# Performance work log

Hardware: AMD Instinct MI355X
Metric: run time of the kernel (lower is better)

The kernel has to match this reference:

```python
import jax, jax.numpy as jnp
import numpy as np

D_MODEL = 2048
N_HEADS = 16
HEAD_DIM = D_MODEL // N_HEADS
LN_EPS = 1e-6  # flax.linen.LayerNorm default
NEG_INF = float('-inf')


def _layernorm_scale_only(x, scale):
    # flax LayerNorm with use_bias=False: normalize over last axis, scale only
    mean = jnp.mean(x, axis=-1, keepdims=True)
    var = jnp.var(x, axis=-1, keepdims=True)
    return (x - mean) * jax.lax.rsqrt(var + LN_EPS) * scale


def setup_inputs() -> dict:
    key = jax.random.key(0)
    ks = jax.random.split(key, 4)
    B, S = 2, 2048
    x = jax.random.normal(ks[0], (B, S, D_MODEL), dtype=jnp.float32)
    Wqkv = jax.random.normal(ks[1], (D_MODEL, 3 * D_MODEL), dtype=jnp.float32) * 0.02
    q_ln_scale = jnp.ones((D_MODEL,), dtype=jnp.float32)
    k_ln_scale = jnp.ones((D_MODEL,), dtype=jnp.float32)
    out_W = jax.random.normal(ks[2], (D_MODEL, D_MODEL), dtype=jnp.float32) * 0.02
    return {"x": x, "Wqkv": Wqkv, "q_ln_scale": q_ln_scale,
            "k_ln_scale": k_ln_scale, "out_W": out_W}


def reference(x, Wqkv, q_ln_scale, k_ln_scale, out_W):
    B, S, _ = x.shape
    qkv = jnp.einsum('bsd,de->bse', x, Wqkv)  # [B,S,3*D] (no bias)
    q, k, v = jnp.split(qkv, 3, axis=-1)
    # QK LayerNorm (attn_qk_ln=True, no bias)
    q = _layernorm_scale_only(q, q_ln_scale)
    k = _layernorm_scale_only(k, k_ln_scale)
    # split heads: [B,S,H,Dh]
    q = q.reshape(B, S, N_HEADS, HEAD_DIM)
    k = k.reshape(B, S, N_HEADS, HEAD_DIM)
    v = v.reshape(B, S, N_HEADS, HEAD_DIM)
    # scaled scores [B,H,S,S]
    scores = jnp.einsum('bshd,bthd->bhst', q / jnp.sqrt(jnp.float32(HEAD_DIM)), k)
    # causal mask: triu(ones, k=1) marks strictly-future positions -> -inf
    causal = jnp.triu(jnp.ones((S, S), dtype=bool), 1)
    scores = jnp.where(causal, NEG_INF, scores)
    # kv-cache mask: arange(S) < S - past_position - S = 0 -> all False (no-op
    # with past_position=0 and no layer_past), faithfully omitted.
    attn = jax.nn.softmax(scores, axis=-1)
    ctx = jnp.einsum('bhst,bthd->bshd', attn, v)  # [B,S,H,Dh]
    out = jnp.einsum('bsd,de->bse', ctx.reshape(B, S, D_MODEL), out_W)
    return out
```

## Files before the change

kernel.cpp:

```cpp
#include <hip/hip_runtime.h>


typedef float f32x4 __attribute__((ext_vector_type(4)));
typedef short s16x8 __attribute__((ext_vector_type(8)));
typedef short s16x4 __attribute__((ext_vector_type(4)));

static __device__ __forceinline__ unsigned short f2bf(float f) {
  unsigned u = __builtin_bit_cast(unsigned, f);
  unsigned r = u + 0x7fffu + ((u >> 16) & 1u);
  return (unsigned short)(r >> 16);
}
static __device__ __forceinline__ float bf2f(unsigned short s) {
  unsigned u = ((unsigned)s) << 16;
  return __builtin_bit_cast(float, u);
}

static __device__ __forceinline__ void gload_lds16(const unsigned short* g, unsigned short* l) {
  __builtin_amdgcn_global_load_lds((const __attribute__((address_space(1))) void*)g,
                                   (__attribute__((address_space(3))) void*)l, 16, 0, 0);
}

__global__ __launch_bounds__(256) void k_cvt4(const float4* __restrict__ in,
                                              s16x4* __restrict__ out, int n) {
  int i = blockIdx.x * 256 + threadIdx.x;
  if (i >= n) return;
  float4 v = in[i];
  s16x4 o = { (short)f2bf(v.x), (short)f2bf(v.y), (short)f2bf(v.z), (short)f2bf(v.w) };
  out[i] = o;
}

__global__ __launch_bounds__(256) void k_twT(const float* __restrict__ in,
                                             unsigned short* __restrict__ out,
                                             int K, int N) {
  __shared__ float tile[32][33];
  const int n0 = blockIdx.x * 32, k0 = blockIdx.y * 32;
  const int tx = threadIdx.x & 31, ty = threadIdx.x >> 5;
#pragma unroll
  for (int rr = 0; rr < 4; ++rr) {
    int kr = ty + rr * 8;
    tile[kr][tx] = in[(size_t)(k0 + kr) * N + n0 + tx];
  }
  __syncthreads();
#pragma unroll
  for (int rr = 0; rr < 4; ++rr) {
    int nr = ty + rr * 8;
    out[(size_t)(n0 + nr) * K + k0 + tx] = f2bf(tile[tx][nr]);
  }
}

template <int BF16OUT>
__global__ __launch_bounds__(256) void k_gemm(const unsigned short* __restrict__ A,
                                              const unsigned short* __restrict__ Bt,
                                              void* __restrict__ Cout,
                                              int M, int N, int K) {
  __shared__ unsigned short sA[128 * 32];
  __shared__ unsigned short sB[128 * 32];
  const int t = threadIdx.x;
  const int w = t >> 6, lane = t & 63, g = lane >> 4, l15 = lane & 15;
  const int m0 = blockIdx.y * 128, n0 = blockIdx.x * 128;
  const int wm = (w >> 1) * 64, wn = (w & 1) * 64;
  f32x4 acc[4][4];
#pragma unroll
  for (int i = 0; i < 4; i++)
#pragma unroll
    for (int j = 0; j < 4; j++) acc[i][j] = (f32x4){0.f, 0.f, 0.f, 0.f};

  const int nk = K >> 5;
  for (int kt = 0; kt < nk; ++kt) {
    __syncthreads();
#pragma unroll
    for (int it = 0; it < 2; ++it) {
      int flat = it * 256 + t;
      int row = flat >> 2, ch = flat & 3;
      gload_lds16(A  + (size_t)(m0 + row) * K + kt * 32 + ch * 8,
                  sA + (size_t)(it * 256 + w * 64) * 8);
      gload_lds16(Bt + (size_t)(n0 + row) * K + kt * 32 + ch * 8,
                  sB + (size_t)(it * 256 + w * 64) * 8);
    }
    __syncthreads();
    s16x8 af[4], bf[4];
#pragma unroll
    for (int i = 0; i < 4; i++) {
      af[i] = *(const s16x8*)&sA[(wm + i * 16 + l15) * 32 + 8 * g];
      bf[i] = *(const s16x8*)&sB[(wn + i * 16 + l15) * 32 + 8 * g];
    }
#pragma unroll
    for (int i = 0; i < 4; i++)
#pragma unroll
      for (int j = 0; j < 4; j++)
        acc[i][j] = __builtin_amdgcn_mfma_f32_16x16x32_bf16(af[i], bf[j], acc[i][j], 0, 0, 0);
  }
#pragma unroll
  for (int i = 0; i < 4; i++) {
#pragma unroll
    for (int j = 0; j < 4; j++) {
#pragma unroll
      for (int r = 0; r < 4; r++) {
        int row = m0 + wm + i * 16 + 4 * g + r;
        int col = n0 + wn + j * 16 + l15;
        if (BF16OUT)
          ((unsigned short*)Cout)[(size_t)row * N + col] = f2bf(acc[i][j][r]);
        else
          ((float*)Cout)[(size_t)row * N + col] = acc[i][j][r];
      }
    }
  }
}

__global__ __launch_bounds__(256) void k_ln(unsigned short* __restrict__ qkv,
                                            const float* __restrict__ qsc,
                                            const float* __restrict__ ksc) {
  __shared__ float red[8];
  const int t = threadIdx.x;
  const int w = t >> 6;
  unsigned short* base = qkv + (size_t)blockIdx.x * 6144;
#pragma unroll
  for (int part = 0; part < 2; ++part) {
    unsigned short* p = base + part * 2048 + t * 8;
    s16x8 v = *(const s16x8*)p;
    float f[8], s = 0.f, q = 0.f;
#pragma unroll
    for (int j = 0; j < 8; j++) { f[j] = bf2f((unsigned short)v[j]); s += f[j]; q += f[j] * f[j]; }
#pragma unroll
    for (int m = 1; m < 64; m <<= 1) { s += __shfl_xor(s, m); q += __shfl_xor(q, m); }
    __syncthreads();
    if ((t & 63) == 0) { red[w] = s; red[4 + w] = q; }
    __syncthreads();
    s = red[0] + red[1] + red[2] + red[3];
    q = red[4] + red[5] + red[6] + red[7];
    float mean = s * (1.f / 2048.f);
    float var = q * (1.f / 2048.f) - mean * mean;
    float inv = rsqrtf(var + 1e-6f);
    const float* sc = part ? ksc : qsc;
    float extra = part ? 1.0f : 0.12751743f;
    s16x8 o;
#pragma unroll
    for (int j = 0; j < 8; j++) o[j] = (short)f2bf((f[j] - mean) * inv * (sc[t * 8 + j] * extra));
    *(s16x8*)p = o;
  }
}

__global__ __launch_bounds__(256) void k_vT(const unsigned short* __restrict__ qkv,
                                            unsigned short* __restrict__ vt) {
  __shared__ unsigned short tl[64][136];
  const int bh = blockIdx.y;
  const int b = bh >> 4, h = bh & 15;
  const int s0 = blockIdx.x * 64;
  const int t = threadIdx.x;
#pragma unroll
  for (int it = 0; it < 4; ++it) {
    int flat = it * 256 + t;
    int r = flat >> 4, c = flat & 15;
    s16x8 v = *(const s16x8*)(qkv + (size_t)(b * 2048 + s0 + r) * 6144 + 4096 + h * 128 + c * 8);
    *((s16x8*)&tl[r][c * 8]) = v;
  }
  __syncthreads();
#pragma unroll
  for (int it = 0; it < 4; ++it) {
    int flat = it * 256 + t;
    int d = flat >> 3, cs = flat & 7;
    s16x8 o;
#pragma unroll
    for (int e = 0; e < 8; e++) {
      int key = (cs >> 2) * 32 + (e >> 2) * 16 + (cs & 3) * 4 + (e & 3);
      o[e] = (short)tl[key][d];
    }
    *(s16x8*)(vt + (size_t)(bh * 128 + d) * 2048 + s0 + cs * 8) = o;
  }
}

__global__ __launch_bounds__(256) void k_attn(const unsigned short* __restrict__ qkv,
                                              const unsigned short* __restrict__ vt,
                                              unsigned short* __restrict__ ctx) {
  __shared__ unsigned short sK[2][64 * 128];
  __shared__ unsigned short sV[2][128 * 64];
  const int t = threadIdx.x;
  const int w = t >> 6, lane = t & 63, g = lane >> 4, l15 = lane & 15;
  const int pair = blockIdx.x, h = blockIdx.y, b = blockIdx.z;
  const int qt0 = 31 - pair, qt1 = pair;
  const int n0 = qt0 + 1;
  const int NT = 33;
  const unsigned short* kbase = qkv + (size_t)(b * 2048) * 6144 + 2048 + h * 128;
  const unsigned short* vbase = vt + (size_t)((b * 16 + h) * 128) * 2048;

  auto issue_kv = [&](int k0, int bufi) {
#pragma unroll
    for (int it2 = 0; it2 < 4; ++it2) {
      int flat = it2 * 256 + t;
      int r = flat >> 4, c = flat & 15;
      gload_lds16(kbase + (size_t)(k0 + r) * 6144 + ((c ^ (r & 15)) * 8),
                  (unsigned short*)&sK[bufi][(it2 * 256 + w * 64) * 8]);
    }
#pragma unroll
    for (int it2 = 0; it2 < 4; ++it2) {
      int flat = it2 * 256 + t;
      int d = flat >> 3, z = flat & 7;
      gload_lds16(vbase + (size_t)d * 2048 + k0 + ((z ^ (d & 7)) * 8),
                  (unsigned short*)&sV[bufi][(it2 * 256 + w * 64) * 8]);
    }
  };

  s16x8 bq[4];
  auto load_q = [&](int q0) {
#pragma unroll
    for (int ks = 0; ks < 4; ++ks)
      bq[ks] = *(const s16x8*)(qkv + (size_t)(b * 2048 + q0 + w * 16 + l15) * 6144 +
                               h * 128 + (ks * 4 + g) * 8);
  };

  f32x4 o[8];
  float mrun, lrun;
  auto reset_state = [&]() {
#pragma unroll
    for (int nd = 0; nd < 8; ++nd) o[nd] = (f32x4){0.f, 0.f, 0.f, 0.f};
    mrun = -INFINITY; lrun = 0.f;
  };
  auto write_o = [&](int q0) {
    float ivr[4];
#pragma unroll
    for (int r = 0; r < 4; ++r) ivr[r] = 1.0f / __shfl(lrun, 4 * g + r);
#pragma unroll
    for (int nd = 0; nd < 8; ++nd) {
      const int col = h * 128 + nd * 16 + l15;
#pragma unroll
      for (int r = 0; r < 4; ++r) {
        const int row = b * 2048 + q0 + w * 16 + 4 * g + r;
        ctx[(size_t)row * 2048 + col] = f2bf(o[nd][r] * ivr[r]);
      }
    }
  };

  reset_state();
  load_q(qt0 * 64);
  issue_kv(0, 0);
  int cur = 0;

  for (int it = 0; it < NT; ++it) {
    const int seg = (it < n0) ? 0 : 1;
    const int qt = seg ? qt1 : qt0;
    const int kt = seg ? it - n0 : it;

    if (it + 1 < NT) {
      const int kn = (it + 1 < n0) ? it + 1 : it + 1 - n0;
      issue_kv(kn * 64, cur ^ 1);
      asm volatile("s_waitcnt vmcnt(8)" ::: "memory");
    } else {
      asm volatile("s_waitcnt vmcnt(0)" ::: "memory");
    }
    __builtin_amdgcn_sched_barrier(0);
    __builtin_amdgcn_s_barrier();

    if (seg == 1 && kt == 0) {
      write_o(qt0 * 64);
      reset_state();
      load_q(qt1 * 64);
    }

    const unsigned short* sKc = &sK[cur][0];
    const unsigned short* sVc = &sV[cur][0];

    f32x4 st[4];
#pragma unroll
    for (int mi = 0; mi < 4; ++mi) st[mi] = (f32x4){0.f, 0.f, 0.f, 0.f};
#pragma unroll
    for (int mi = 0; mi < 4; ++mi) {
#pragma unroll
      for (int ks = 0; ks < 4; ++ks) {
        s16x8 ak = *(const s16x8*)&sKc[(mi * 16 + l15) * 128 + (((ks * 4 + g) ^ l15) * 8)];
        st[mi] = __builtin_amdgcn_mfma_f32_16x16x32_bf16(ak, bq[ks], st[mi], 0, 0, 0);
      }
    }

    if (kt == qt) {
      const int qloc = w * 16 + l15;
#pragma unroll
      for (int mi = 0; mi < 4; ++mi)
#pragma unroll
        for (int r = 0; r < 4; ++r)
          if (mi * 16 + 4 * g + r > qloc) st[mi][r] = -INFINITY;
    }

    float mt = -INFINITY;
#pragma unroll
    for (int mi = 0; mi < 4; ++mi)
#pragma unroll
      for (int r = 0; r < 4; ++r) mt = fmaxf(mt, st[mi][r]);
    mt = fmaxf(mt, __shfl_xor(mt, 16));
    mt = fmaxf(mt, __shfl_xor(mt, 32));

    if (!__all(mt <= mrun + 8.f)) {
      const float mnew = fmaxf(mrun, mt);
      const float alpha = exp2f(mrun - mnew);
      lrun *= alpha;
      float ar[4];
#pragma unroll
      for (int r = 0; r < 4; ++r) ar[r] = __shfl(alpha, 4 * g + r);
#pragma unroll
      for (int nd = 0; nd < 8; ++nd)
#pragma unroll
        for (int r = 0; r < 4; ++r) o[nd][r] *= ar[r];
      mrun = mnew;
    }

    float ls = 0.f;
#pragma unroll
    for (int mi = 0; mi < 4; ++mi)
#pragma unroll
      for (int r = 0; r < 4; ++r) {
        float pp = exp2f(st[mi][r] - mrun);
        st[mi][r] = pp;
        ls += pp;
      }
    ls += __shfl_xor(ls, 16);
    ls += __shfl_xor(ls, 32);
    lrun += ls;

    s16x8 pa01, pa23;
#pragma unroll
    for (int j = 0; j < 8; ++j) {
      pa01[j] = (short)f2bf(st[j >> 2][j & 3]);
      pa23[j] = (short)f2bf(st[2 + (j >> 2)][j & 3]);
    }

#pragma unroll
    for (int nd = 0; nd < 8; ++nd) {
      const int d = nd * 16 + l15;
      const int zs = d & 7;
      s16x8 bv0 = *(const s16x8*)&sVc[d * 64 + ((g ^ zs) * 8)];
      s16x8 bv1 = *(const s16x8*)&sVc[d * 64 + (((4 + g) ^ zs) * 8)];
      o[nd] = __builtin_amdgcn_mfma_f32_16x16x32_bf16(pa01, bv0, o[nd], 0, 0, 0);
      o[nd] = __builtin_amdgcn_mfma_f32_16x16x32_bf16(pa23, bv1, o[nd], 0, 0, 0);
    }

    __builtin_amdgcn_sched_barrier(0);
    __builtin_amdgcn_s_barrier();
    cur ^= 1;
  }
  write_o(qt1 * 64);
}

extern "C" void kernel_launch(void* const* d_in, const int* in_sizes, int n_in,
                              void* d_out, int out_size, void* d_ws, size_t ws_size,
                              hipStream_t stream) {
  (void)in_sizes; (void)n_in; (void)out_size; (void)ws_size;
  const float* x    = (const float*)d_in[0];
  const float* Wqkv = (const float*)d_in[1];
  const float* qsc  = (const float*)d_in[2];
  const float* ksc  = (const float*)d_in[3];
  const float* outW = (const float*)d_in[4];

  char* ws = (char*)d_ws;
  unsigned short* xb  = (unsigned short*)(ws);
  unsigned short* wT  = (unsigned short*)(ws + 16777216);
  unsigned short* owT = (unsigned short*)(ws + 41943040);
  unsigned short* qkv = (unsigned short*)(ws + 50331648);
  unsigned short* vt  = (unsigned short*)(ws + 100663296);
  unsigned short* ctx = xb;

  k_cvt4<<<8192, 256, 0, stream>>>((const float4*)x, (s16x4*)xb, 2097152);
  k_twT<<<dim3(192, 64), 256, 0, stream>>>(Wqkv, wT, 2048, 6144);
  k_twT<<<dim3(64, 64), 256, 0, stream>>>(outW, owT, 2048, 2048);
  k_gemm<1><<<dim3(48, 32), 256, 0, stream>>>(xb, wT, (void*)qkv, 4096, 6144, 2048);
  k_ln<<<4096, 256, 0, stream>>>(qkv, qsc, ksc);
  k_vT<<<dim3(32, 32), 256, 0, stream>>>(qkv, vt);
  k_attn<<<dim3(16, 16, 2), 256, 0, stream>>>(qkv, vt, ctx);
  k_gemm<0><<<dim3(16, 32), 256, 0, stream>>>(ctx, owT, d_out, 4096, 2048, 2048);
}
```

Measured before the change: 317.2 us.

## Replace QKV projection GEMM with 256x256 tiled, 8-wave pipelined MFMA kernel

Adds a new bf16 GEMM kernel for the QKV projection. It uses 256x256 output tiles, 512 threads, double-buffered 64-wide K stages loaded directly into XOR-swizzled LDS, and interleaved quarter-tile MFMA phases with explicit waitcnt, barriers and setprio. An XCD-aware block swizzle remaps the 384 blocks. The goal is more data reuse per LDS load and overlap of global loads with compute, replacing the 128x128 kernel. The cost is heavy register pressure and fragile hand-tuned vmcnt counts.

After: 303.1 us. -4.5%, faster.

```diff
diff --git a/kernel.cpp b/kernel.cpp
--- a/kernel.cpp
+++ b/kernel.cpp
@@ -46,6 +46,165 @@
     int nr = ty + rr * 8;
     out[(size_t)(n0 + nr) * K + k0 + tx] = f2bf(tile[tx][nr]);
   }
+}
+
+__global__ __launch_bounds__(512, 2) void k_gemm256(const unsigned short* __restrict__ A,
+                                                    const unsigned short* __restrict__ Bt,
+                                                    unsigned short* __restrict__ Cout,
+                                                    int N, int K, int nbn) {
+  __shared__ unsigned short sA[2 * 2 * 128 * 64];
+  __shared__ unsigned short sB[2 * 2 * 128 * 64];
+  const int t = threadIdx.x;
+  const int wid = t >> 6, lane = t & 63, g = lane >> 4, l15 = lane & 15;
+  const int wm2 = wid >> 2, wn2 = wid & 3;
+  const int xr = l15 & 7;
+
+  const int cpx = (int)gridDim.x >> 3;
+  const int swz = ((int)blockIdx.x & 7) * cpx + ((int)blockIdx.x >> 3);
+  const int m0 = (swz / nbn) * 256, n0 = (swz % nbn) * 256;
+
+  const int srow = t >> 3;
+  const int sslot = (t & 7) ^ (srow & 7);
+  const unsigned short* pA = A  + (size_t)(m0 + srow) * K + sslot * 8;
+  const unsigned short* pB = Bt + (size_t)(n0 + srow) * K + sslot * 8;
+  const int ldsb = wid * 512;
+
+  auto stageA = [&](int kt, int h) {
+#pragma unroll
+    for (int j = 0; j < 2; ++j)
+      gload_lds16(pA + (size_t)(h * 128 + j * 64) * K + kt * 64,
+                  sA + ((kt & 1) * 2 + h) * 8192 + j * 4096 + ldsb);
+  };
+  auto stageB = [&](int kt, int h) {
+#pragma unroll
+    for (int j = 0; j < 2; ++j)
+      gload_lds16(pB + (size_t)(h * 128 + j * 64) * K + kt * 64,
+                  sB + ((kt & 1) * 2 + h) * 8192 + j * 4096 + ldsb);
+  };
+
+  const int arow = wm2 * 64 + l15;
+  const int brow = wn2 * 32 + l15;
+  const int sl0 = (g ^ xr) * 8, sl1 = ((4 + g) ^ xr) * 8;
+
+  f32x4 acc[2][2][4][2];
+#pragma unroll
+  for (int a = 0; a < 2; ++a)
+#pragma unroll
+    for (int b = 0; b < 2; ++b)
+#pragma unroll
+      for (int c = 0; c < 4; ++c)
+#pragma unroll
+        for (int d = 0; d < 2; ++d) acc[a][b][c][d] = (f32x4){0.f, 0.f, 0.f, 0.f};
+
+  const int NK = K >> 6;
+  stageA(0, 0); stageB(0, 0); stageB(0, 1); stageA(0, 1); stageA(1, 0); stageB(1, 0);
+  asm volatile("s_waitcnt vmcnt(6)" ::: "memory");
+  __builtin_amdgcn_sched_barrier(0);
+  asm volatile("s_barrier" ::: "memory");
+
+  for (int s = 0; s < NK; ++s) {
+    const unsigned short* aT = sA + (s & 1) * 16384;
+    const unsigned short* bT = sB + (s & 1) * 16384;
+    const bool tail = (s >= NK - 2);
+    s16x8 af[4][2], bf0[2][2], bf1[2][2];
+
+#pragma unroll
+    for (int fm = 0; fm < 4; ++fm) {
+      af[fm][0] = *(const s16x8*)&aT[(arow + fm * 16) * 64 + sl0];
+      af[fm][1] = *(const s16x8*)&aT[(arow + fm * 16) * 64 + sl1];
+    }
+#pragma unroll
+    for (int fn = 0; fn < 2; ++fn) {
+      bf0[fn][0] = *(const s16x8*)&bT[(brow + fn * 16) * 64 + sl0];
+      bf0[fn][1] = *(const s16x8*)&bT[(brow + fn * 16) * 64 + sl1];
+    }
+    if (s + 1 < NK) stageB(s + 1, 1);
+    asm volatile("s_barrier" ::: "memory");
+    __builtin_amdgcn_s_setprio(1);
+#pragma unroll
+    for (int fm = 0; fm < 4; ++fm)
+#pragma unroll
+      for (int fn = 0; fn < 2; ++fn)
+#pragma unroll
+        for (int ks = 0; ks < 2; ++ks)
+          acc[0][0][fm][fn] = __builtin_amdgcn_mfma_f32_16x16x32_bf16(
+              af[fm][ks], bf0[fn][ks], acc[0][0][fm][fn], 0, 0, 0);
+    __builtin_amdgcn_s_setprio(0);
+    asm volatile("s_barrier" ::: "memory");
+
+#pragma unroll
+    for (int fn = 0; fn < 2; ++fn) {
+      bf1[fn][0] = *(const s16x8*)&bT[8192 + (brow + fn * 16) * 64 + sl0];
+      bf1[fn][1] = *(const s16x8*)&bT[8192 + (brow + fn * 16) * 64 + sl1];
+    }
+    if (s + 1 < NK) stageA(s + 1, 1);
+    if (tail) asm volatile("s_waitcnt vmcnt(0)" ::: "memory");
+    else      asm volatile("s_waitcnt vmcnt(8)" ::: "memory");
+    __builtin_amdgcn_sched_barrier(0);
+    asm volatile("s_barrier" ::: "memory");
+    __builtin_amdgcn_s_setprio(1);
+#pragma unroll
+    for (int fm = 0; fm < 4; ++fm)
+#pragma unroll
+      for (int fn = 0; fn < 2; ++fn)
+#pragma unroll
+        for (int ks = 0; ks < 2; ++ks)
+          acc[0][1][fm][fn] = __builtin_amdgcn_mfma_f32_16x16x32_bf16(
+              af[fm][ks], bf1[fn][ks], acc[0][1][fm][fn], 0, 0, 0);
+    __builtin_amdgcn_s_setprio(0);
+    asm volatile("s_barrier" ::: "memory");
+
+#pragma unroll
+    for (int fm = 0; fm < 4; ++fm) {
+      af[fm][0] = *(const s16x8*)&aT[8192 + (arow + fm * 16) * 64 + sl0];
+      af[fm][1] = *(const s16x8*)&aT[8192 + (arow + fm * 16) * 64 + sl1];
+    }
+    if (s + 2 < NK) stageA(s + 2, 0);
+    asm volatile("s_barrier" ::: "memory");
+    __builtin_amdgcn_s_setprio(1);
+#pragma unroll
+    for (int fm = 0; fm < 4; ++fm)
+#pragma unroll
+      for (int fn = 0; fn < 2; ++fn)
+#pragma unroll
+        for (int ks = 0; ks < 2; ++ks)
+          acc[1][0][fm][fn] = __builtin_amdgcn_mfma_f32_16x16x32_bf16(
+              af[fm][ks], bf0[fn][ks], acc[1][0][fm][fn], 0, 0, 0);
+    __builtin_amdgcn_s_setprio(0);
+    asm volatile("s_barrier" ::: "memory");
+
+    if (s + 2 < NK) stageB(s + 2, 0);
+    if (tail) asm volatile("s_waitcnt vmcnt(0)" ::: "memory");
+    else      asm volatile("s_waitcnt vmcnt(6)" ::: "memory");
+    __builtin_amdgcn_sched_barrier(0);
+    asm volatile("s_barrier" ::: "memory");
+    __builtin_amdgcn_s_setprio(1);
+#pragma unroll
+    for (int fm = 0; fm < 4; ++fm)
+#pragma unroll
+      for (int fn = 0; fn < 2; ++fn)
+#pragma unroll
+        for (int ks = 0; ks < 2; ++ks)
+          acc[1][1][fm][fn] = __builtin_amdgcn_mfma_f32_16x16x32_bf16(
+              af[fm][ks], bf1[fn][ks], acc[1][1][fm][fn], 0, 0, 0);
+    __builtin_amdgcn_s_setprio(0);
+    asm volatile("s_barrier" ::: "memory");
+  }
+
+#pragma unroll
+  for (int qm = 0; qm < 2; ++qm)
+#pragma unroll
+    for (int qn = 0; qn < 2; ++qn)
+#pragma unroll
+      for (int fm = 0; fm < 4; ++fm)
+#pragma unroll
+        for (int fn = 0; fn < 2; ++fn)
+#pragma unroll
+          for (int r = 0; r < 4; ++r) {
+            const int row = m0 + qm * 128 + wm2 * 64 + fm * 16 + g * 4 + r;
+            const int col = n0 + qn * 128 + wn2 * 32 + fn * 16 + l15;
+            Cout[(size_t)row * N + col] = f2bf(acc[qm][qn][fm][fn][r]);
+          }
 }
 
 template <int BF16OUT>
@@ -360,7 +519,7 @@
   k_cvt4<<<8192, 256, 0, stream>>>((const float4*)x, (s16x4*)xb, 2097152);
   k_twT<<<dim3(192, 64), 256, 0, stream>>>(Wqkv, wT, 2048, 6144);
   k_twT<<<dim3(64, 64), 256, 0, stream>>>(outW, owT, 2048, 2048);
-  k_gemm<1><<<dim3(48, 32), 256, 0, stream>>>(xb, wT, (void*)qkv, 4096, 6144, 2048);
+  k_gemm256<<<384, 512, 0, stream>>>(xb, wT, qkv, 6144, 2048, 24);
   k_ln<<<4096, 256, 0, stream>>>(qkv, qsc, ksc);
   k_vT<<<dim3(32, 32), 256, 0, stream>>>(qkv, vt);
   k_attn<<<dim3(16, 16, 2), 256, 0, stream>>>(qkv, vt, ctx);
```

## Replace GEMM with double-buffered 128x256 tile kernel using swizzled LDS

Applied to the files above, without the earlier changes.

Replaces the simple single-buffered 128x128 GEMM with a 512-thread kernel computing 128x256 tiles at K-step 64. Global-to-LDS loads are double-buffered and overlapped with MFMA work through split half-tile stages and explicit vmcnt waits. The LDS layout uses XOR swizzling to avoid bank conflicts, and the block index is remapped for cache locality. It also raises MFMA wave priority around the compute sections. The cost is higher LDS use and register pressure, plus hand-placed barriers that must stay correct.

After: 280.8 us. 11.5% less time.

```diff
diff --git a/kernel.cpp b/kernel.cpp
--- a/kernel.cpp
+++ b/kernel.cpp
@@ -49,62 +49,128 @@
 }
 
 template <int BF16OUT>
-__global__ __launch_bounds__(256) void k_gemm(const unsigned short* __restrict__ A,
-                                              const unsigned short* __restrict__ Bt,
-                                              void* __restrict__ Cout,
-                                              int M, int N, int K) {
-  __shared__ unsigned short sA[128 * 32];
-  __shared__ unsigned short sB[128 * 32];
+__global__ __launch_bounds__(512, 2) void k_g8p(const unsigned short* __restrict__ A,
+                                                const unsigned short* __restrict__ Bt,
+                                                void* __restrict__ Cout,
+                                                int N, int K, int nbn) {
+  __shared__ unsigned short sA[2 * 128 * 64];
+  __shared__ unsigned short sB[2 * 2 * 128 * 64];
   const int t = threadIdx.x;
-  const int w = t >> 6, lane = t & 63, g = lane >> 4, l15 = lane & 15;
-  const int m0 = blockIdx.y * 128, n0 = blockIdx.x * 128;
-  const int wm = (w >> 1) * 64, wn = (w & 1) * 64;
-  f32x4 acc[4][4];
-#pragma unroll
-  for (int i = 0; i < 4; i++)
-#pragma unroll
-    for (int j = 0; j < 4; j++) acc[i][j] = (f32x4){0.f, 0.f, 0.f, 0.f};
-
-  const int nk = K >> 5;
-  for (int kt = 0; kt < nk; ++kt) {
-    __syncthreads();
-#pragma unroll
-    for (int it = 0; it < 2; ++it) {
-      int flat = it * 256 + t;
-      int row = flat >> 2, ch = flat & 3;
-      gload_lds16(A  + (size_t)(m0 + row) * K + kt * 32 + ch * 8,
-                  sA + (size_t)(it * 256 + w * 64) * 8);
-      gload_lds16(Bt + (size_t)(n0 + row) * K + kt * 32 + ch * 8,
-                  sB + (size_t)(it * 256 + w * 64) * 8);
-    }
-    __syncthreads();
-    s16x8 af[4], bf[4];
-#pragma unroll
-    for (int i = 0; i < 4; i++) {
-      af[i] = *(const s16x8*)&sA[(wm + i * 16 + l15) * 32 + 8 * g];
-      bf[i] = *(const s16x8*)&sB[(wn + i * 16 + l15) * 32 + 8 * g];
-    }
-#pragma unroll
-    for (int i = 0; i < 4; i++)
-#pragma unroll
-      for (int j = 0; j < 4; j++)
-        acc[i][j] = __builtin_amdgcn_mfma_f32_16x16x32_bf16(af[i], bf[j], acc[i][j], 0, 0, 0);
-  }
-#pragma unroll
-  for (int i = 0; i < 4; i++) {
-#pragma unroll
-    for (int j = 0; j < 4; j++) {
-#pragma unroll
-      for (int r = 0; r < 4; r++) {
-        int row = m0 + wm + i * 16 + 4 * g + r;
-        int col = n0 + wn + j * 16 + l15;
-        if (BF16OUT)
-          ((unsigned short*)Cout)[(size_t)row * N + col] = f2bf(acc[i][j][r]);
-        else
-          ((float*)Cout)[(size_t)row * N + col] = acc[i][j][r];
-      }
-    }
-  }
+  const int wid = t >> 6, lane = t & 63, g = lane >> 4, l15 = lane & 15;
+  const int wm2 = wid >> 2, wn2 = wid & 3;
+  const int xr = l15 & 7;
+
+  const int cpx = (int)gridDim.x >> 3;
+  const int swz = ((int)blockIdx.x & 7) * cpx + ((int)blockIdx.x >> 3);
+  const int m0 = (swz / nbn) * 128, n0 = (swz % nbn) * 256;
+
+  const int srow = t >> 3;
+  const int sslot = (t & 7) ^ (srow & 7);
+  const unsigned short* pA = A  + (size_t)(m0 + srow) * K + sslot * 8;
+  const unsigned short* pB = Bt + (size_t)(n0 + srow) * K + sslot * 8;
+
+  auto stageA = [&](int kt) {
+#pragma unroll
+    for (int j = 0; j < 2; ++j)
+      gload_lds16(pA + (size_t)(j * 64) * K + kt * 64,
+                  sA + (kt & 1) * 8192 + j * 4096 + t * 8);
+  };
+  auto stageB = [&](int kt, int h) {
+#pragma unroll
+    for (int j = 0; j < 2; ++j)
+      gload_lds16(pB + (size_t)(h * 128 + j * 64) * K + kt * 64,
+                  sB + (kt & 1) * 16384 + h * 8192 + j * 4096 + t * 8);
+  };
+
+  const int sl0 = (g ^ xr) * 8, sl1 = ((4 + g) ^ xr) * 8;
+  const int arow = wm2 * 64 + l15;
+  const int brow = wn2 * 32 + l15;
+
+  f32x4 acc[2][4][2];
+#pragma unroll
+  for (int h = 0; h < 2; ++h)
+#pragma unroll
+    for (int fm = 0; fm < 4; ++fm)
+#pragma unroll
+      for (int fn = 0; fn < 2; ++fn) acc[h][fm][fn] = (f32x4){0.f, 0.f, 0.f, 0.f};
+
+  const int NK = K >> 6;
+  stageA(0); stageB(0, 0); stageB(0, 1);
+  asm volatile("s_waitcnt vmcnt(2)" ::: "memory");
+  __builtin_amdgcn_sched_barrier(0);
+  asm volatile("s_barrier" ::: "memory");
+
+  for (int s = 0; s < NK; ++s) {
+    const unsigned short* aT = sA + (s & 1) * 8192;
+    const unsigned short* bT = sB + (s & 1) * 16384;
+    const bool tail = (s == NK - 1);
+    s16x8 af[4][2], bfr[2][2];
+
+#pragma unroll
+    for (int fm = 0; fm < 4; ++fm) {
+      af[fm][0] = *(const s16x8*)&aT[(arow + fm * 16) * 64 + sl0];
+      af[fm][1] = *(const s16x8*)&aT[(arow + fm * 16) * 64 + sl1];
+    }
+#pragma unroll
+    for (int fn = 0; fn < 2; ++fn) {
+      bfr[fn][0] = *(const s16x8*)&bT[(brow + fn * 16) * 64 + sl0];
+      bfr[fn][1] = *(const s16x8*)&bT[(brow + fn * 16) * 64 + sl1];
+    }
+    if (!tail) { stageA(s + 1); stageB(s + 1, 0); }
+    if (tail) asm volatile("s_waitcnt vmcnt(0)" ::: "memory");
+    else      asm volatile("s_waitcnt vmcnt(4)" ::: "memory");
+    __builtin_amdgcn_sched_barrier(0);
+    asm volatile("s_barrier" ::: "memory");
+    __builtin_amdgcn_s_setprio(1);
+#pragma unroll
+    for (int fm = 0; fm < 4; ++fm)
+#pragma unroll
+      for (int fn = 0; fn < 2; ++fn)
+#pragma unroll
+        for (int ks = 0; ks < 2; ++ks)
+          acc[0][fm][fn] = __builtin_amdgcn_mfma_f32_16x16x32_bf16(
+              af[fm][ks], bfr[fn][ks], acc[0][fm][fn], 0, 0, 0);
+    __builtin_amdgcn_s_setprio(0);
+    asm volatile("s_barrier" ::: "memory");
+
+#pragma unroll
+    for (int fn = 0; fn < 2; ++fn) {
+      bfr[fn][0] = *(const s16x8*)&bT[8192 + (brow + fn * 16) * 64 + sl0];
+      bfr[fn][1] = *(const s16x8*)&bT[8192 + (brow + fn * 16) * 64 + sl1];
+    }
+    if (!tail) stageB(s + 1, 1);
+    if (tail) asm volatile("s_waitcnt vmcnt(0)" ::: "memory");
+    else      asm volatile("s_waitcnt vmcnt(2)" ::: "memory");
+    __builtin_amdgcn_sched_barrier(0);
+    asm volatile("s_barrier" ::: "memory");
+    __builtin_amdgcn_s_setprio(1);
+#pragma unroll
+    for (int fm = 0; fm < 4; ++fm)
+#pragma unroll
+      for (int fn = 0; fn < 2; ++fn)
+#pragma unroll
+        for (int ks = 0; ks < 2; ++ks)
+          acc[1][fm][fn] = __builtin_amdgcn_mfma_f32_16x16x32_bf16(
+              af[fm][ks], bfr[fn][ks], acc[1][fm][fn], 0, 0, 0);
+    __builtin_amdgcn_s_setprio(0);
+    asm volatile("s_barrier" ::: "memory");
+  }
+
+#pragma unroll
+  for (int h = 0; h < 2; ++h)
+#pragma unroll
+    for (int fm = 0; fm < 4; ++fm)
+#pragma unroll
+      for (int fn = 0; fn < 2; ++fn)
+#pragma unroll
+        for (int r = 0; r < 4; ++r) {
+          const int row = m0 + wm2 * 64 + fm * 16 + g * 4 + r;
+          const int col = n0 + h * 128 + wn2 * 32 + fn * 16 + l15;
+          if (BF16OUT)
+            ((unsigned short*)Cout)[(size_t)row * N + col] = f2bf(acc[h][fm][fn][r]);
+          else
+            ((float*)Cout)[(size_t)row * N + col] = acc[h][fm][fn][r];
+        }
 }
 
 __global__ __launch_bounds__(256) void k_ln(unsigned short* __restrict__ qkv,
@@ -360,9 +426,9 @@
   k_cvt4<<<8192, 256, 0, stream>>>((const float4*)x, (s16x4*)xb, 2097152);
   k_twT<<<dim3(192, 64), 256, 0, stream>>>(Wqkv, wT, 2048, 6144);
   k_twT<<<dim3(64, 64), 256, 0, stream>>>(outW, owT, 2048, 2048);
-  k_gemm<1><<<dim3(48, 32), 256, 0, stream>>>(xb, wT, (void*)qkv, 4096, 6144, 2048);
+  k_g8p<1><<<768, 512, 0, stream>>>(xb, wT, qkv, 6144, 2048, 24);
   k_ln<<<4096, 256, 0, stream>>>(qkv, qsc, ksc);
   k_vT<<<dim3(32, 32), 256, 0, stream>>>(qkv, vt);
   k_attn<<<dim3(16, 16, 2), 256, 0, stream>>>(qkv, vt, ctx);
-  k_gemm<0><<<dim3(16, 32), 256, 0, stream>>>(ctx, owT, d_out, 4096, 2048, 2048);
-}
+  k_g8p<0><<<256, 512, 0, stream>>>(ctx, owT, d_out, 2048, 2048, 8);
+}
```
